# Optimization experiments

Measured on AMD Instinct MI355X. Metric: run time of the kernel, lower is better.

The kernel has to match this reference:

```python
import jax, jax.numpy as jnp
import numpy as np

N, E, D, DH, MH, MO = 100000, 1600000, 128, 512, 512, 128
EPS_BN = 1e-5
EPS_LN = 1e-5


def setup_inputs() -> dict:
    key = jax.random.key(0)
    ks = jax.random.split(key, 16)
    def lin(k, fan_in, shape):
        return jax.random.normal(k, shape, jnp.float32) / np.sqrt(fan_in)
    return {
        'x': jax.random.normal(ks[0], (N, D), jnp.float32),
        'src': jax.random.randint(ks[1], (E,), 0, N, jnp.int32),
        'dst': jax.random.randint(ks[2], (E,), 0, N, jnp.int32),
        'gcn_w': lin(ks[3], D, (D, D)),
        'gcn_b': jnp.zeros((D,), jnp.float32),
        'ff_w1': lin(ks[4], D, (D, DH)),
        'ff_b1': jnp.zeros((DH,), jnp.float32),
        'ln_g': jnp.ones((DH,), jnp.float32),
        'ln_b': jnp.zeros((DH,), jnp.float32),
        'ff_w2': lin(ks[5], DH, (DH, D)),
        'ff_b2': jnp.zeros((D,), jnp.float32),
        'fc1_w': lin(ks[6], D, (D, MH)),
        'fc1_b': jnp.zeros((MH,), jnp.float32),
        'bn1_g': jnp.ones((MH,), jnp.float32),
        'bn1_b': jnp.zeros((MH,), jnp.float32),
        'fc2_w': lin(ks[7], MH, (MH, MH)),
        'fc2_b': jnp.zeros((MH,), jnp.float32),
        'bn2_g': jnp.ones((MH,), jnp.float32),
        'bn2_b': jnp.zeros((MH,), jnp.float32),
        'fc3_w': lin(ks[8], MH, (MH, MO)),
        'fc3_b': jnp.zeros((MO,), jnp.float32),
        'bn3_g': jnp.ones((MO,), jnp.float32),
        'bn3_b': jnp.zeros((MO,), jnp.float32),
        'fc4_w': lin(ks[9], MO, (MO, 1)),
        'fc4_b': jnp.zeros((1,), jnp.float32),
    }


def _gelu(x):
    return jax.nn.gelu(x, approximate=False)  # torch nn.GELU default (erf)


def _batchnorm(x, g, b):
    # BatchNorm1d in training mode: batch statistics, biased variance
    m = jnp.mean(x, axis=0)
    v = jnp.var(x, axis=0)
    return (x - m) * jax.lax.rsqrt(v + EPS_BN) * g + b


def reference(x, src, dst, gcn_w, gcn_b, ff_w1, ff_b1, ln_g, ln_b, ff_w2, ff_b2,
              fc1_w, fc1_b, bn1_g, bn1_b, fc2_w, fc2_b, bn2_g, bn2_b,
              fc3_w, fc3_b, bn3_g, bn3_b, fc4_w, fc4_b):
    n = x.shape[0]
    ones = jnp.ones(src.shape[0], x.dtype)
    out_deg = jnp.clip(jax.ops.segment_sum(ones, src, num_segments=n), 1.0)
    in_deg = jnp.clip(jax.ops.segment_sum(ones, dst, num_segments=n), 1.0)
    # GraphConv, norm='both': left-normalize, aggregate, matmul (in==out), right-normalize, bias
    h = x * (out_deg ** -0.5)[:, None]
    agg = jax.ops.segment_sum(h[src], dst, num_segments=n)  # [N, D]
    h = agg @ gcn_w
    h = h * (in_deg ** -0.5)[:, None] + gcn_b
    # FeedForwardLayer: lin1 -> GELU -> LayerNorm -> lin2
    f = _gelu(h @ ff_w1 + ff_b1)
    mu = jnp.mean(f, axis=-1, keepdims=True)
    var = jnp.var(f, axis=-1, keepdims=True)
    f = (f - mu) * jax.lax.rsqrt(var + EPS_LN) * ln_g + ln_b
    h = f @ ff_w2 + ff_b2  # [N, D]
    # MLP head
    h = _batchnorm(_gelu(h @ fc1_w + fc1_b), bn1_g, bn1_b)
    h = _batchnorm(_gelu(h @ fc2_w + fc2_b), bn2_g, bn2_b)
    h = _batchnorm(_gelu(h @ fc3_w + fc3_b), bn3_g, bn3_b)
    return h @ fc4_w + fc4_b  # [N, 1]
```

## Files before the change

### kernel.cpp

```cpp
#include <hip/hip_runtime.h>
#include <hip/hip_bf16.h>

#define N_NODES 100000
#define NPAD    100096
#define NRB     782
#define E_EDGES 1600000
#define NBLK_SCAN 98

#define HNR  4
#define HP   64
#define HCHK 25000
#define HRSZ 32768

#define NBK  196
#define PCHK 6250

#define AS1 __attribute__((address_space(1)))
#define AS3 __attribute__((address_space(3)))

typedef unsigned int   uint;
typedef unsigned short ushort;
typedef __attribute__((ext_vector_type(8))) short bfx8;
typedef __attribute__((ext_vector_type(4))) float fx4;

__device__ __forceinline__ float bf2f(ushort u) {
    return __uint_as_float(((uint)u) << 16);
}
__device__ __forceinline__ ushort f2bf(float f) {
    uint x = __float_as_uint(f);
    return (ushort)((x + 0x7FFFu + ((x >> 16) & 1u)) >> 16);
}
__device__ __forceinline__ float gelu_fast(float x) {
    float u = 1.5957691f * __builtin_fmaf(0.044715f * x * x, x, x);
    return x / (1.0f + __expf(-u));
}
__device__ __forceinline__ float wave_sum(float v) {
    #pragma unroll
    for (int m = 1; m < 64; m <<= 1) v += __shfl_xor(v, m, 64);
    return v;
}
__device__ __forceinline__ int xcd_swz(int orig, int nwg) {
    int q = nwg >> 3, r = nwg & 7;
    int x = orig & 7, o = orig >> 3;
    return (x < r ? x * (q + 1) : r * (q + 1) + (x - r) * q) + o;
}

__global__ void k_hist(const int* __restrict__ idx, uint* __restrict__ part)
{
    __shared__ uint h[HRSZ / 2];
    int c = blockIdx.x & (HP - 1);
    int r = blockIdx.x / HP;
    int t = threadIdx.x;
    for (int i = t; i < HRSZ / 2; i += 256) h[i] = 0u;
    __syncthreads();
    int base = r << 15;
    int e0 = c * HCHK;
    for (int e = e0 + t; e < e0 + HCHK; e += 256) {
        int v = idx[e] - base;
        if ((uint)v < (uint)HRSZ)
            atomicAdd(&h[v >> 1], 1u << ((v & 1) * 16));
    }
    __syncthreads();
    uint* dst = part + ((size_t)blockIdx.x << 14);
    for (int i = t; i < HRSZ / 2; i += 256) dst[i] = h[i];
}

__global__ void k_degmerge(const uint* __restrict__ partO, const uint* __restrict__ partI,
                           int* __restrict__ inc, float* __restrict__ oscale,
                           float* __restrict__ ininv)
{
    int n = blockIdx.x * 256 + threadIdx.x;
    if (n >= NPAD) return;
    int r = n >> 15, i = (n & 32767) >> 1, hi = (n & 1) * 16;
    const uint* po = partO + ((size_t)(r * HP) << 14) + i;
    const uint* pi = partI + ((size_t)(r * HP) << 14) + i;
    uint so = 0, si = 0;
    for (int c = 0; c < HP; ++c) {
        so += (po[(size_t)c << 14] >> hi) & 0xffffu;
        si += (pi[(size_t)c << 14] >> hi) & 0xffffu;
    }
    inc[n] = (int)si;
    oscale[n] = rsqrtf((float)max((int)so, 1));
    ininv[n] = rsqrtf((float)max((int)si, 1));
}

__global__ void k_scan1(const int* __restrict__ inc, int* __restrict__ coff, int* __restrict__ btot)
{
    __shared__ int a[1024], bsh[1024];
    int t = threadIdx.x;
    int i = blockIdx.x * 1024 + t;
    a[t] = (i < N_NODES) ? inc[i] : 0;
    __syncthreads();
    int* s = a; int* d = bsh;
    for (int dd = 1; dd < 1024; dd <<= 1) {
        int v = s[t] + ((t >= dd) ? s[t - dd] : 0);
        d[t] = v;
        __syncthreads();
        int* tmp = s; s = d; d = tmp;
    }
    if (i < N_NODES) coff[i + 1] = s[t];
    if (t == 1023) btot[blockIdx.x] = s[t];
}

__global__ void k_scan2(int* __restrict__ btot)
{
    __shared__ int a[128], bsh[128];
    int t = threadIdx.x;
    a[t] = (t < NBLK_SCAN) ? btot[t] : 0;
    __syncthreads();
    int* s = a; int* d = bsh;
    for (int dd = 1; dd < 128; dd <<= 1) {
        int v = s[t] + ((t >= dd) ? s[t - dd] : 0);
        d[t] = v;
        __syncthreads();
        int* tmp = s; s = d; d = tmp;
    }
    if (t < NBLK_SCAN) btot[t] = s[t];
}

__global__ void k_scan3(int* __restrict__ coff, const int* __restrict__ btot)
{
    int i = blockIdx.x * 256 + threadIdx.x;
    if (i == 0) coff[0] = 0;
    if (i < N_NODES) {
        int blk = i >> 10;
        if (blk > 0) coff[i + 1] += btot[blk - 1];
    }
}

__global__ void k_curinit(const int* __restrict__ coff, int* __restrict__ gcur)
{
    int t = threadIdx.x;
    if (t < NBK) gcur[t] = coff[t << 9];
}

__global__ __launch_bounds__(256) void k_part(const int* __restrict__ src, const int* __restrict__ dst,
                                              int* __restrict__ gcur, uint* __restrict__ tmp)
{
    __shared__ int cnt[NBK], rcnt[NBK], base[NBK], loff[NBK];
    __shared__ int sa[256], sb[256];
    __shared__ uint arr[PCHK];
    int t = threadIdx.x;
    if (t < NBK) { cnt[t] = 0; rcnt[t] = 0; }
    __syncthreads();
    int e0 = blockIdx.x * PCHK;
    for (int e = e0 + t; e < e0 + PCHK; e += 256)
        atomicAdd(&cnt[dst[e] >> 9], 1);
    __syncthreads();
    sa[t] = (t < NBK) ? cnt[t] : 0;
    __syncthreads();
    int* s = sa; int* d = sb;
    for (int dd = 1; dd < 256; dd <<= 1) {
        int v = s[t] + ((t >= dd) ? s[t - dd] : 0);
        d[t] = v;
        __syncthreads();
        int* w = s; s = d; d = w;
    }
    if (t < NBK) {
        loff[t] = s[t] - cnt[t];
        base[t] = atomicAdd(&gcur[t], cnt[t]);
    }
    __syncthreads();
    for (int e = e0 + t; e < e0 + PCHK; e += 256) {
        int dv = dst[e];
        int b = dv >> 9;
        int r = atomicAdd(&rcnt[b], 1);
        arr[loff[b] + r] = ((uint)src[e] << 9) | (uint)(dv & 511);
    }
    __syncthreads();
    for (int b = 0; b < NBK; ++b) {
        int n = cnt[b], lo = loff[b], gb = base[b];
        for (int i = t; i < n; i += 256)
            tmp[gb + i] = arr[lo + i];
    }
}

__global__ __launch_bounds__(256) void k_fill2(const uint* __restrict__ tmp, const int* __restrict__ coff,
                                               int* __restrict__ eidx)
{
    __shared__ int lco[512];
    __shared__ int lcnt[512];
    int b = blockIdx.x, t = threadIdx.x;
    int n0 = b << 9;
    for (int i = t; i < 512; i += 256) {
        int node = n0 + i;
        lco[i] = (node <= N_NODES) ? coff[node] : E_EDGES;
        lcnt[i] = 0;
    }
    __syncthreads();
    int s0 = coff[n0];
    int s1 = (n0 + 512 <= N_NODES) ? coff[n0 + 512] : E_EDGES;
    for (int e = s0 + t; e < s1; e += 256) {
        uint v = tmp[e];
        int dl = v & 511;
        int r = atomicAdd(&lcnt[dl], 1);
        eidx[lco[dl] + r] = (int)(v >> 9);
    }
}

__global__ void k_xhat(const float* __restrict__ x, const float* __restrict__ oscale,
                       ushort* __restrict__ xh)
{
    size_t i = (size_t)blockIdx.x * 256 + threadIdx.x;
    size_t e0 = i * 4;
    int row = (int)(e0 >> 7);
    uint2 o;
    if (row < N_NODES) {
        float4 v = *(const float4*)(x + e0);
        float s = oscale[row];
        o.x = (uint)f2bf(v.x * s) | ((uint)f2bf(v.y * s) << 16);
        o.y = (uint)f2bf(v.z * s) | ((uint)f2bf(v.w * s) << 16);
    } else {
        o.x = 0u; o.y = 0u;
    }
    *(uint2*)(xh + e0) = o;
}

__global__ void k_agg(const int* __restrict__ off, const int* __restrict__ eidx,
                      const ushort* __restrict__ xh, ushort* __restrict__ agg)
{
    int wid = threadIdx.x >> 6, lane = threadIdx.x & 63;
    int r = blockIdx.x * 4 + wid;
    if (r >= NPAD) return;
    int f = lane & 15;
    int g = lane >> 4;
    float a[8] = {0.f, 0.f, 0.f, 0.f, 0.f, 0.f, 0.f, 0.f};
    if (r < N_NODES) {
        int s = off[r], e = off[r + 1];
        for (int i = s + g; i < e; i += 4) {
            int sv = eidx[i];
            bfx8 v = *(const bfx8*)(xh + (size_t)sv * 128 + f * 8);
            #pragma unroll
            for (int k = 0; k < 8; ++k) a[k] += bf2f((ushort)v[k]);
        }
    }
    #pragma unroll
    for (int k = 0; k < 8; ++k) {
        a[k] += __shfl_xor(a[k], 16, 64);
        a[k] += __shfl_xor(a[k], 32, 64);
    }
    if (g == 0) {
        bfx8 o;
        #pragma unroll
        for (int k = 0; k < 8; ++k) o[k] = (short)f2bf(a[k]);
        *(bfx8*)(agg + (size_t)r * 128 + f * 8) = o;
    }
}

__global__ void k_wT(const float* __restrict__ W, int K, int M, ushort* __restrict__ Wt)
{
    int id = blockIdx.x * 256 + threadIdx.x;
    if (id < K * M) {
        int m = id / K, k = id - m * K;
        Wt[id] = f2bf(W[(size_t)k * M + m]);
    }
}

__global__ void k_wT_ln(const float* __restrict__ W, const float* __restrict__ g,
                        const float* __restrict__ b, const float* __restrict__ b2,
                        ushort* __restrict__ Wt, float* __restrict__ u, float* __restrict__ t)
{
    int wid = threadIdx.x >> 6, lane = threadIdx.x & 63;
    int m = blockIdx.x * 4 + wid;
    if (m >= 128) return;
    float us = 0.f, ts = 0.f;
    for (int k = lane; k < 512; k += 64) {
        float w = W[(size_t)k * 128 + m];
        float gk = g[k], bk = b[k];
        Wt[(size_t)m * 512 + k] = f2bf(gk * w);
        us += gk * w; ts += bk * w;
    }
    us = wave_sum(us); ts = wave_sum(ts);
    if (lane == 0) { u[m] = us; t[m] = ts + b2[m]; }
}

template <int K1, int EPI1, int STATS2>
__global__ __launch_bounds__(256, 2) void k_fused(
    const ushort* __restrict__ A1, const ushort* __restrict__ B1t,
    const ushort* __restrict__ B2t, ushort* __restrict__ C,
    const float* __restrict__ c1v0, const float* __restrict__ r1v0,
    const float* __restrict__ r1v1, const float* __restrict__ c1v1,
    const float* __restrict__ bias2,
    float* __restrict__ lnS, float* __restrict__ lnC,
    float* __restrict__ pS, float* __restrict__ pQ)
{
    __shared__ __align__(16) char smem[32768 + 32768 + 2048];
    char* A2 = smem;
    char* S  = smem + 32768;
    float* st_s = (float*)(smem + 65536);
    float* st_q = (float*)(smem + 65536 + 1024);

    const int rb = xcd_swz(blockIdx.x, gridDim.x);
    const int tid = threadIdx.x;
    const int lane = tid & 63;
    const int wid = tid >> 6;
    const int m0 = (wid >> 1) * 64;
    const int n0 = (wid & 1) * 64;
    const int frl = lane & 15;
    const int kg = lane >> 4;

    char* As = S;
    char* Bs = S + 16384;
    fx4 acc[4][4] = {};
    const ushort* Arow0 = A1 + (size_t)(rb * 128) * K1;

    for (int kb = 0; kb < K1; kb += 64) {
        #pragma unroll
        for (int c = 0; c < 4; ++c) {
            int b = c * 4096 + tid * 16;
            int row = b >> 7;
            int cibs = (b & 127) ^ ((row & 7) << 4);
            const char* ga = (const char*)(Arow0 + (size_t)row * K1 + kb) + cibs;
            const char* gb = (const char*)(B1t + (size_t)row * K1 + kb) + cibs;
            char* la = As + c * 4096 + (wid << 10);
            char* lb = Bs + c * 4096 + (wid << 10);
            __builtin_amdgcn_global_load_lds((const AS1 void*)ga, (AS3 void*)la, 16, 0, 0);
            __builtin_amdgcn_global_load_lds((const AS1 void*)gb, (AS3 void*)lb, 16, 0, 0);
        }
        __syncthreads();
        #pragma unroll
        for (int kk = 0; kk < 2; ++kk) {
            bfx8 av[4], bv[4];
            #pragma unroll
            for (int i = 0; i < 4; ++i) {
                int ar = m0 + i * 16 + frl;
                int ab = (ar * 128 + kk * 64 + kg * 16) ^ ((ar & 7) << 4);
                av[i] = *(const bfx8*)(As + ab);
                int br = n0 + i * 16 + frl;
                int bb = (br * 128 + kk * 64 + kg * 16) ^ ((br & 7) << 4);
                bv[i] = *(const bfx8*)(Bs + bb);
            }
            #pragma unroll
            for (int i = 0; i < 4; ++i)
                #pragma unroll
                for (int j = 0; j < 4; ++j)
                    acc[i][j] = __builtin_amdgcn_mfma_f32_16x16x32_bf16(av[i], bv[j], acc[i][j], 0, 0, 0);
        }
        __syncthreads();
    }

    #pragma unroll
    for (int j = 0; j < 4; ++j) {
        int colL = n0 + j * 16 + frl;
        float c0 = c1v0[colL];
        float c1 = (EPI1 == 3) ? c1v1[colL] : 0.f;
        #pragma unroll
        for (int i = 0; i < 4; ++i) {
            int rbaseL = m0 + i * 16 + kg * 4;
            #pragma unroll
            for (int r = 0; r < 4; ++r) {
                float v = acc[i][j][r];
                int rowL = rbaseL + r;
                int grow = rb * 128 + rowL;
                if (EPI1 == 0) v = v * r1v0[grow] + c0;
                else           v = r1v0[grow] * v + r1v1[grow] * c1 + c0;
                *(ushort*)(A2 + rowL * 256 + ((colL * 2) ^ ((rowL & 7) << 4))) = f2bf(v);
            }
        }
    }
    __syncthreads();

    float rs = 0.f, rq = 0.f;
    const int rowR = tid >> 1, halfR = tid & 1;

    for (int cb2 = 0; cb2 < 4; ++cb2) {
        #pragma unroll
        for (int c = 0; c < 8; ++c) {
            int b = c * 4096 + tid * 16;
            int row = b >> 8;
            int cibs = (b & 255) ^ ((row & 7) << 4);
            const char* gb = (const char*)(B2t + (size_t)(cb2 * 128 + row) * 128) + cibs;
            char* lb = S + c * 4096 + (wid << 10);
            __builtin_amdgcn_global_load_lds((const AS1 void*)gb, (AS3 void*)lb, 16, 0, 0);
        }
        __syncthreads();

        fx4 a2[4][4] = {};
        #pragma unroll
        for (int kk = 0; kk < 4; ++kk) {
            bfx8 av[4], bv[4];
            int c2 = kk * 64 + kg * 16;
            #pragma unroll
            for (int i = 0; i < 4; ++i) {
                int ar = m0 + i * 16 + frl;
                av[i] = *(const bfx8*)(A2 + ar * 256 + (c2 ^ ((ar & 7) << 4)));
                int br = n0 + i * 16 + frl;
                bv[i] = *(const bfx8*)(S + br * 256 + (c2 ^ ((br & 7) << 4)));
            }
            #pragma unroll
            for (int i = 0; i < 4; ++i)
                #pragma unroll
                for (int j = 0; j < 4; ++j)
                    a2[i][j] = __builtin_amdgcn_mfma_f32_16x16x32_bf16(av[i], bv[j], a2[i][j], 0, 0, 0);
        }
        __syncthreads();

        float sL[4] = {0.f, 0.f, 0.f, 0.f}, qL[4] = {0.f, 0.f, 0.f, 0.f};
        #pragma unroll
        for (int j = 0; j < 4; ++j) {
            int colL = n0 + j * 16 + frl;
            float bcol = bias2[cb2 * 128 + colL];
            #pragma unroll
            for (int i = 0; i < 4; ++i) {
                int rbaseL = m0 + i * 16 + kg * 4;
                #pragma unroll
                for (int r = 0; r < 4; ++r) {
                    float v = gelu_fast(a2[i][j][r] + bcol);
                    int rowL = rbaseL + r;
                    if (STATS2 == 1) {
                        if (rb * 128 + rowL < N_NODES) { sL[j] += v; qL[j] += v * v; }
                    }
                    *(ushort*)(S + rowL * 256 + ((colL * 2) ^ ((rowL & 7) << 4))) = f2bf(v);
                }
            }
            if (STATS2 == 1) {
                float s = sL[j], q = qL[j];
                s += __shfl_xor(s, 16, 64); s += __shfl_xor(s, 32, 64);
                q += __shfl_xor(q, 16, 64); q += __shfl_xor(q, 32, 64);
                if (kg == 0) {
                    st_s[(wid >> 1) * 128 + n0 + j * 16 + frl] = s;
                    st_q[(wid >> 1) * 128 + n0 + j * 16 + frl] = q;
                }
            }
        }
        __syncthreads();

        {
            int r2 = tid >> 4;
            int s2 = tid & 15;
            #pragma unroll
            for (int pass = 0; pass < 8; ++pass) {
                int rowL = pass * 16 + r2;
                int boff = rowL * 256 + ((s2 * 16) ^ ((rowL & 7) << 4));
                bfx8 v = *(const bfx8*)(S + boff);
                *(bfx8*)((char*)(C + (size_t)(rb * 128 + rowL) * 512 + cb2 * 128) + s2 * 16) = v;
            }
        }
        if (STATS2 == 1 && tid < 128) {
            size_t pidx = ((size_t)rb * 4 + cb2) * 128 + tid;
            pS[pidx] = st_s[tid] + st_s[128 + tid];
            pQ[pidx] = st_q[tid] + st_q[128 + tid];
        }
        if (STATS2 == 2) {
            #pragma unroll
            for (int ss = 0; ss < 8; ++ss) {
                int boff = rowR * 256 + (((halfR * 64 + ss * 8) * 2) ^ ((rowR & 7) << 4));
                bfx8 v = *(const bfx8*)(S + boff);
                #pragma unroll
                for (int k2 = 0; k2 < 8; ++k2) {
                    float f = bf2f((ushort)v[k2]);
                    rs += f; rq += f * f;
                }
            }
        }
        __syncthreads();
    }

    if (STATS2 == 2) {
        rs += __shfl_xor(rs, 1, 64);
        rq += __shfl_xor(rq, 1, 64);
        if (halfR == 0) {
            float mean = rs * (1.f / 512.f);
            float var = fmaxf(rq * (1.f / 512.f) - mean * mean, 0.f);
            float sr = rsqrtf(var + 1e-5f);
            int grow = rb * 128 + rowR;
            lnS[grow] = sr;
            lnC[grow] = -mean * sr;
        }
    }
}

template <int EPI, int STATS>
__global__ __launch_bounds__(256, 4) void k_gemm(
    const ushort* __restrict__ A, const ushort* __restrict__ Bt,
    ushort* __restrict__ C, int K, int M,
    const float* __restrict__ colv0, const float* __restrict__ rowv0,
    float* __restrict__ pS, float* __restrict__ pQ, int grb0)
{
    __shared__ __align__(16) char smem[32768 + (STATS == 1 ? 1024 : 0)];
    char* AsB = smem;
    char* BsB = smem + 16384;

    const int nwg = gridDim.x;
    const int wgid = xcd_swz(blockIdx.x, nwg);
    const int nCB = M >> 7;
    const int cb = wgid % nCB;
    const int rb = wgid / nCB;
    const int tid = threadIdx.x;
    const int lane = tid & 63;
    const int wid = tid >> 6;
    const int m0 = (wid >> 1) * 64;
    const int n0 = (wid & 1) * 64;
    const int frl = lane & 15;
    const int kg = lane >> 4;

    float* statsf = (float*)(smem + 32768);
    if (STATS == 1 && tid < 128) { statsf[tid] = 0.f; statsf[128 + tid] = 0.f; }

    fx4 acc[4][4] = {};

    const ushort* Arow0 = A + (size_t)(rb * 128) * K;
    const ushort* Brow0 = Bt + (size_t)(cb * 128) * K;

    for (int kb = 0; kb < K; kb += 64) {
        #pragma unroll
        for (int c = 0; c < 4; ++c) {
            int b = c * 4096 + tid * 16;
            int row = b >> 7;
            int cibs = (b & 127) ^ ((row & 7) << 4);
            const char* ga = (const char*)(Arow0 + (size_t)row * K + kb) + cibs;
            const char* gb = (const char*)(Brow0 + (size_t)row * K + kb) + cibs;
            char* la = AsB + c * 4096 + (wid << 10);
            char* lb = BsB + c * 4096 + (wid << 10);
            __builtin_amdgcn_global_load_lds((const AS1 void*)ga, (AS3 void*)la, 16, 0, 0);
            __builtin_amdgcn_global_load_lds((const AS1 void*)gb, (AS3 void*)lb, 16, 0, 0);
        }
        __syncthreads();
        #pragma unroll
        for (int kk = 0; kk < 2; ++kk) {
            bfx8 av[4], bv[4];
            #pragma unroll
            for (int i = 0; i < 4; ++i) {
                int ar = m0 + i * 16 + frl;
                int ab = (ar * 128 + kk * 64 + kg * 16) ^ ((ar & 7) << 4);
                av[i] = *(const bfx8*)(AsB + ab);
                int br = n0 + i * 16 + frl;
                int bb = (br * 128 + kk * 64 + kg * 16) ^ ((br & 7) << 4);
                bv[i] = *(const bfx8*)(BsB + bb);
            }
            #pragma unroll
            for (int i = 0; i < 4; ++i)
                #pragma unroll
                for (int j = 0; j < 4; ++j)
                    acc[i][j] = __builtin_amdgcn_mfma_f32_16x16x32_bf16(av[i], bv[j], acc[i][j], 0, 0, 0);
        }
        __syncthreads();
    }

    float sL[4] = {0.f, 0.f, 0.f, 0.f}, qL[4] = {0.f, 0.f, 0.f, 0.f};
    #pragma unroll
    for (int j = 0; j < 4; ++j) {
        int colL = n0 + j * 16 + frl;
        float c0 = colv0[cb * 128 + colL];
        #pragma unroll
        for (int i = 0; i < 4; ++i) {
            int rbaseL = m0 + i * 16 + kg * 4;
            #pragma unroll
            for (int r = 0; r < 4; ++r) {
                float v = acc[i][j][r];
                int rowL = rbaseL + r;
                int grow = (grb0 + rb) * 128 + rowL;
                if (EPI == 0) v = v * rowv0[grow] + c0;
                else          v = gelu_fast(v + c0);
                if (STATS == 1) {
                    if (grow < N_NODES) { sL[j] += v; qL[j] += v * v; }
                }
                int boff = rowL * 256 + ((colL * 2) ^ ((rowL & 7) << 4));
                *(ushort*)(smem + boff) = f2bf(v);
            }
        }
    }
    if (STATS == 1) {
        #pragma unroll
        for (int j = 0; j < 4; ++j) {
            float s = sL[j], q = qL[j];
            s += __shfl_xor(s, 16, 64); s += __shfl_xor(s, 32, 64);
            q += __shfl_xor(q, 16, 64); q += __shfl_xor(q, 32, 64);
            if (kg == 0) {
                atomicAdd(&statsf[n0 + j * 16 + frl], s);
                atomicAdd(&statsf[128 + n0 + j * 16 + frl], q);
            }
        }
    }
    __syncthreads();
    {
        int r2 = tid >> 4;
        int s2 = tid & 15;
        #pragma unroll
        for (int pass = 0; pass < 8; ++pass) {
            int rowL = pass * 16 + r2;
            int boff = rowL * 256 + ((s2 * 16) ^ ((rowL & 7) << 4));
            bfx8 v = *(const bfx8*)(smem + boff);
            *(bfx8*)((char*)(C + (size_t)(rb * 128 + rowL) * M + cb * 128) + s2 * 16) = v;
        }
    }
    if (STATS == 1 && tid < 128) {
        size_t pidx = ((size_t)(grb0 + rb) * nCB + cb) * 128 + tid;
        pS[pidx] = statsf[tid];
        pQ[pidx] = statsf[128 + tid];
    }
}

__global__ void k_colmerge(const float* __restrict__ pS, const float* __restrict__ pQ,
                           float* __restrict__ oS, float* __restrict__ oQ, int M)
{
    int wid = threadIdx.x >> 6, lane = threadIdx.x & 63;
    int m = blockIdx.x * 4 + wid;
    if (m >= M) return;
    int nCB = M >> 7, cb = m >> 7, colL = m & 127;
    float s = 0.f, q = 0.f;
    for (int rb = lane; rb < NRB; rb += 64) {
        size_t idx = ((size_t)rb * nCB + cb) * 128 + colL;
        s += pS[idx]; q += pQ[idx];
    }
    s = wave_sum(s); q = wave_sum(q);
    if (lane == 0) { oS[m] = s; oQ[m] = q; }
}

__global__ void k_fold(const float* __restrict__ W, const float* __restrict__ bw,
                       const float* __restrict__ g, const float* __restrict__ bb,
                       const float* __restrict__ sum, const float* __restrict__ sqs,
                       int K, int M, ushort* __restrict__ WtO, float* __restrict__ bO)
{
    int wid = threadIdx.x >> 6, lane = threadIdx.x & 63;
    int m = blockIdx.x * 4 + wid;
    if (m >= M) return;
    float acc = 0.f;
    for (int k = lane; k < K; k += 64) {
        float mean = sum[k] * (1.f / (float)N_NODES);
        float var = sqs[k] * (1.f / (float)N_NODES) - mean * mean;
        float s = g[k] * rsqrtf(var + 1e-5f);
        float t = bb[k] - mean * s;
        float w = W[(size_t)k * M + m];
        WtO[(size_t)m * K + k] = f2bf(w * s);
        acc += t * w;
    }
    acc = wave_sum(acc);
    if (lane == 0) bO[m] = bw[m] + acc;
}

__global__ void k_out(const ushort* __restrict__ m3, const ushort* __restrict__ w4,
                      const float* __restrict__ b4, float* __restrict__ out)
{
    int wid = threadIdx.x >> 6, lane = threadIdx.x & 63;
    int r = blockIdx.x * 4 + wid;
    if (r >= N_NODES) return;
    uint u = *(const uint*)(m3 + (size_t)r * 128 + lane * 2);
    uint w = *(const uint*)(w4 + lane * 2);
    float acc = bf2f((ushort)(u & 0xffffu)) * bf2f((ushort)(w & 0xffffu))
              + bf2f((ushort)(u >> 16)) * bf2f((ushort)(w >> 16));
    acc = wave_sum(acc);
    if (lane == 0) out[r] = acc + b4[0];
}

extern "C" void kernel_launch(void* const* d_in, const int* in_sizes, int n_in,
                              void* d_out, int out_size, void* d_ws, size_t ws_size,
                              hipStream_t stream)
{
    const float* x     = (const float*)d_in[0];
    const int*   src   = (const int*)d_in[1];
    const int*   dst   = (const int*)d_in[2];
    const float* gcn_w = (const float*)d_in[3];
    const float* gcn_b = (const float*)d_in[4];
    const float* ff_w1 = (const float*)d_in[5];
    const float* ff_b1 = (const float*)d_in[6];
    const float* ln_g  = (const float*)d_in[7];
    const float* ln_b  = (const float*)d_in[8];
    const float* ff_w2 = (const float*)d_in[9];
    const float* ff_b2 = (const float*)d_in[10];
    const float* fc1_w = (const float*)d_in[11];
    const float* fc1_b = (const float*)d_in[12];
    const float* bn1_g = (const float*)d_in[13];
    const float* bn1_b = (const float*)d_in[14];
    const float* fc2_w = (const float*)d_in[15];
    const float* fc2_b = (const float*)d_in[16];
    const float* bn2_g = (const float*)d_in[17];
    const float* bn2_b = (const float*)d_in[18];
    const float* fc3_w = (const float*)d_in[19];
    const float* fc3_b = (const float*)d_in[20];
    const float* bn3_g = (const float*)d_in[21];
    const float* bn3_b = (const float*)d_in[22];
    const float* fc4_w = (const float*)d_in[23];
    const float* fc4_b = (const float*)d_in[24];
    float* out = (float*)d_out;
    (void)in_sizes; (void)n_in; (void)out_size;

    char* base = (char*)d_ws;
    char* p = base;
    auto alloc = [&](size_t bytes) -> char* {
        char* r = p;
        p += (bytes + 255) & ~(size_t)255;
        return r;
    };
    int*    inc    = (int*)alloc((size_t)NPAD * 4);
    int*    coff   = (int*)alloc(((size_t)NPAD + 1) * 4);
    int*    btot   = (int*)alloc(128 * 4);
    int*    gcur   = (int*)alloc(256 * 4);
    int*    eidx   = (int*)alloc((size_t)E_EDGES * 4);
    float*  oscale = (float*)alloc((size_t)NPAD * 4);
    float*  ininv  = (float*)alloc((size_t)NPAD * 4);
    float*  bns    = (float*)alloc(6 * 512 * 4);
    float*  b2p    = (float*)alloc(512 * 4);
    float*  b3p    = (float*)alloc(128 * 4);
    float*  b4p    = (float*)alloc(4);
    float*  lnS    = (float*)alloc((size_t)NPAD * 4);
    float*  lnC    = (float*)alloc((size_t)NPAD * 4);
    float*  lnU    = (float*)alloc(128 * 4);
    float*  lnT    = (float*)alloc(128 * 4);
    float*  pS     = (float*)alloc((size_t)4 * NPAD * 4);
    float*  pQ     = (float*)alloc((size_t)4 * NPAD * 4);
    ushort* gwT    = (ushort*)alloc(128 * 128 * 2);
    ushort* ff1T   = (ushort*)alloc(512 * 128 * 2);
    ushort* ff2T   = (ushort*)alloc(128 * 512 * 2);
    ushort* fc1T   = (ushort*)alloc(512 * 128 * 2);
    ushort* fc2T   = (ushort*)alloc(512 * 512 * 2);
    ushort* fc3T   = (ushort*)alloc(128 * 512 * 2);
    ushort* w4t    = (ushort*)alloc(128 * 2);
    ushort* buf1   = (ushort*)alloc((size_t)NPAD * 128 * 2);
    ushort* bufC   = (ushort*)alloc((size_t)NPAD * 512 * 2);

    size_t used = (size_t)(p - base);
    bool   sep  = (used + (size_t)NPAD * 512 * 2) <= ws_size;
    ushort* m2  = sep ? (ushort*)alloc((size_t)NPAD * 512 * 2) : bufC;

    uint* partO = (uint*)bufC;
    uint* partI = partO + (size_t)HNR * HP * (HRSZ / 2);
    uint* etmp  = (uint*)bufC;
    ushort* xh  = bufC;
    ushort* agg = buf1;

    float* bn1s = bns;
    float* bn1q = bns + 512;
    float* bn2s = bns + 1024;
    float* bn2q = bns + 1536;
    float* bn3s = bns + 2048;
    float* bn3q = bns + 2560;

    k_hist<<<HNR * HP, 256, 0, stream>>>(src, partO);
    k_hist<<<HNR * HP, 256, 0, stream>>>(dst, partI);
    k_degmerge<<<(NPAD + 255) / 256, 256, 0, stream>>>(partO, partI, inc, oscale, ininv);
    k_scan1<<<NBLK_SCAN, 1024, 0, stream>>>(inc, coff, btot);
    k_scan2<<<1, 128, 0, stream>>>(btot);
    k_scan3<<<(N_NODES + 255) / 256, 256, 0, stream>>>(coff, btot);
    k_curinit<<<1, 256, 0, stream>>>(coff, gcur);
    k_part<<<E_EDGES / PCHK, 256, 0, stream>>>(src, dst, gcur, etmp);
    k_fill2<<<NBK, 256, 0, stream>>>(etmp, coff, eidx);
    k_xhat<<<(NPAD / 256) * 32, 256, 0, stream>>>(x, oscale, xh);
    k_agg<<<NPAD / 4, 256, 0, stream>>>(coff, eidx, xh, agg);

    k_wT<<<(128 * 128) / 256, 256, 0, stream>>>(gcn_w, 128, 128, gwT);
    k_wT<<<(128 * 512) / 256, 256, 0, stream>>>(ff_w1, 128, 512, ff1T);
    k_wT<<<(128 * 512) / 256, 256, 0, stream>>>(fc1_w, 128, 512, fc1T);
    k_wT_ln<<<32, 256, 0, stream>>>(ff_w2, ln_g, ln_b, ff_b2, ff2T, lnU, lnT);

    k_fused<128, 0, 2><<<NRB, 256, 0, stream>>>(agg, gwT, ff1T, bufC,
                                                gcn_b, ininv, nullptr, nullptr, ff_b1,
                                                lnS, lnC, nullptr, nullptr);
    k_fused<512, 3, 1><<<NRB, 256, 0, stream>>>(bufC, ff2T, fc1T, bufC,
                                                lnT, lnS, lnC, lnU, fc1_b,
                                                nullptr, nullptr, pS, pQ);
    k_colmerge<<<128, 256, 0, stream>>>(pS, pQ, bn1s, bn1q, 512);
    k_fold<<<512 / 4, 256, 0, stream>>>(fc2_w, fc2_b, bn1_g, bn1_b, bn1s, bn1q, 512, 512, fc2T, b2p);
    if (sep) {
        k_gemm<1, 1><<<4 * NRB, 256, 0, stream>>>(bufC, fc2T, m2, 512, 512,
                                                  b2p, nullptr, pS, pQ, 0);
    } else {
        const int cOff[6] = {0, 195, 390, 585, 780, 782};
        for (int c = 0; c < 5; ++c) {
            int rb0 = cOff[c], nrb = cOff[c + 1] - rb0;
            k_gemm<1, 1><<<nrb * 4, 256, 0, stream>>>(bufC + (size_t)rb0 * 128 * 512, fc2T,
                                                      buf1, 512, 512,
                                                      b2p, nullptr, pS, pQ, rb0);
            hipMemcpyAsync(bufC + (size_t)rb0 * 128 * 512, buf1,
                           (size_t)nrb * 128 * 512 * 2, hipMemcpyDeviceToDevice, stream);
        }
    }
    k_colmerge<<<128, 256, 0, stream>>>(pS, pQ, bn2s, bn2q, 512);
    k_fold<<<128 / 4, 256, 0, stream>>>(fc3_w, fc3_b, bn2_g, bn2_b, bn2s, bn2q, 512, 128, fc3T, b3p);
    k_gemm<1, 1><<<NRB, 256, 0, stream>>>(m2, fc3T, buf1, 512, 128,
                                          b3p, nullptr, pS, pQ, 0);
    k_colmerge<<<32, 256, 0, stream>>>(pS, pQ, bn3s, bn3q, 128);
    k_fold<<<1, 256, 0, stream>>>(fc4_w, fc4_b, bn3_g, bn3_b, bn3s, bn3q, 128, 1, w4t, b4p);
    k_out<<<N_NODES / 4, 256, 0, stream>>>(buf1, w4t, b4p, out);
}
```

Measured before the change: 672.8 us.

## Run fused GEMM kernels with 512 threads and narrower per-wave tiles

Doubles the fused kernel block size to 512 threads (8 waves in a 2x4 layout), so each wave computes a 64x32 output tile instead of 64x64. Loads, epilogue, store and LayerNorm stat loops are re-split across the extra threads. This cuts accumulator registers per wave and puts more waves on each CU to hide latency. The cost is more LDS fragment reads per MFMA, since each wave reloads the A fragments for only half the columns, plus an extra shuffle step in the row reductions.

New measurement: 655.6 us. 1.03x faster.

```diff
diff --git a/kernel.cpp b/kernel.cpp
--- a/kernel.cpp
+++ b/kernel.cpp
@@ -275,7 +275,7 @@
 }
 
 template <int K1, int EPI1, int STATS2>
-__global__ __launch_bounds__(256, 2) void k_fused(
+__global__ __launch_bounds__(512, 4) void k_fused(
     const ushort* __restrict__ A1, const ushort* __restrict__ B1t,
     const ushort* __restrict__ B2t, ushort* __restrict__ C,
     const float* __restrict__ c1v0, const float* __restrict__ r1v0,
@@ -294,64 +294,66 @@
     const int tid = threadIdx.x;
     const int lane = tid & 63;
     const int wid = tid >> 6;
-    const int m0 = (wid >> 1) * 64;
-    const int n0 = (wid & 1) * 64;
+    const int wr = wid >> 2;
+    const int wc = wid & 3;
+    const int m0 = wr * 64;
+    const int n0 = wc * 32;
     const int frl = lane & 15;
     const int kg = lane >> 4;
 
     char* As = S;
     char* Bs = S + 16384;
-    fx4 acc[4][4] = {};
+    fx4 acc[4][2] = {};
     const ushort* Arow0 = A1 + (size_t)(rb * 128) * K1;
 
     for (int kb = 0; kb < K1; kb += 64) {
         #pragma unroll
-        for (int c = 0; c < 4; ++c) {
-            int b = c * 4096 + tid * 16;
+        for (int c = 0; c < 2; ++c) {
+            int b = c * 8192 + tid * 16;
             int row = b >> 7;
             int cibs = (b & 127) ^ ((row & 7) << 4);
             const char* ga = (const char*)(Arow0 + (size_t)row * K1 + kb) + cibs;
             const char* gb = (const char*)(B1t + (size_t)row * K1 + kb) + cibs;
-            char* la = As + c * 4096 + (wid << 10);
-            char* lb = Bs + c * 4096 + (wid << 10);
+            char* la = As + c * 8192 + (wid << 10);
+            char* lb = Bs + c * 8192 + (wid << 10);
             __builtin_amdgcn_global_load_lds((const AS1 void*)ga, (AS3 void*)la, 16, 0, 0);
             __builtin_amdgcn_global_load_lds((const AS1 void*)gb, (AS3 void*)lb, 16, 0, 0);
         }
         __syncthreads();
         #pragma unroll
         for (int kk = 0; kk < 2; ++kk) {
-            bfx8 av[4], bv[4];
+            bfx8 av[4], bv[2];
             #pragma unroll
             for (int i = 0; i < 4; ++i) {
                 int ar = m0 + i * 16 + frl;
-                int ab = (ar * 128 + kk * 64 + kg * 16) ^ ((ar & 7) << 4);
-                av[i] = *(const bfx8*)(As + ab);
-                int br = n0 + i * 16 + frl;
-                int bb = (br * 128 + kk * 64 + kg * 16) ^ ((br & 7) << 4);
-                bv[i] = *(const bfx8*)(Bs + bb);
+                av[i] = *(const bfx8*)(As + ((ar * 128 + kk * 64 + kg * 16) ^ ((ar & 7) << 4)));
+            }
+            #pragma unroll
+            for (int j = 0; j < 2; ++j) {
+                int br = n0 + j * 16 + frl;
+                bv[j] = *(const bfx8*)(Bs + ((br * 128 + kk * 64 + kg * 16) ^ ((br & 7) << 4)));
             }
             #pragma unroll
             for (int i = 0; i < 4; ++i)
                 #pragma unroll
-                for (int j = 0; j < 4; ++j)
+                for (int j = 0; j < 2; ++j)
                     acc[i][j] = __builtin_amdgcn_mfma_f32_16x16x32_bf16(av[i], bv[j], acc[i][j], 0, 0, 0);
         }
         __syncthreads();
     }
 
     #pragma unroll
-    for (int j = 0; j < 4; ++j) {
+    for (int j = 0; j < 2; ++j) {
         int colL = n0 + j * 16 + frl;
         float c0 = c1v0[colL];
         float c1 = (EPI1 == 3) ? c1v1[colL] : 0.f;
         #pragma unroll
         for (int i = 0; i < 4; ++i) {
-            int rbaseL = m0 + i * 16 + kg * 4;
             #pragma unroll
             for (int r = 0; r < 4; ++r) {
+                int rowL = m0 + i * 16 + kg * 4 + r;
+                int grow = rb * 128 + rowL;
                 float v = acc[i][j][r];
-                int rowL = rbaseL + r;
-                int grow = rb * 128 + rowL;
                 if (EPI1 == 0) v = v * r1v0[grow] + c0;
                 else           v = r1v0[grow] * v + r1v1[grow] * c1 + c0;
                 *(ushort*)(A2 + rowL * 256 + ((colL * 2) ^ ((rowL & 7) << 4))) = f2bf(v);
@@ -361,65 +363,67 @@
     __syncthreads();
 
     float rs = 0.f, rq = 0.f;
-    const int rowR = tid >> 1, halfR = tid & 1;
+    const int rowR = tid >> 2;
+    const int qR = tid & 3;
 
     for (int cb2 = 0; cb2 < 4; ++cb2) {
         #pragma unroll
-        for (int c = 0; c < 8; ++c) {
-            int b = c * 4096 + tid * 16;
+        for (int c = 0; c < 4; ++c) {
+            int b = c * 8192 + tid * 16;
             int row = b >> 8;
             int cibs = (b & 255) ^ ((row & 7) << 4);
             const char* gb = (const char*)(B2t + (size_t)(cb2 * 128 + row) * 128) + cibs;
-            char* lb = S + c * 4096 + (wid << 10);
+            char* lb = S + c * 8192 + (wid << 10);
             __builtin_amdgcn_global_load_lds((const AS1 void*)gb, (AS3 void*)lb, 16, 0, 0);
         }
         __syncthreads();
 
-        fx4 a2[4][4] = {};
+        fx4 a2[4][2] = {};
         #pragma unroll
         for (int kk = 0; kk < 4; ++kk) {
-            bfx8 av[4], bv[4];
             int c2 = kk * 64 + kg * 16;
+            bfx8 av[4], bv[2];
             #pragma unroll
             for (int i = 0; i < 4; ++i) {
                 int ar = m0 + i * 16 + frl;
                 av[i] = *(const bfx8*)(A2 + ar * 256 + (c2 ^ ((ar & 7) << 4)));
-                int br = n0 + i * 16 + frl;
-                bv[i] = *(const bfx8*)(S + br * 256 + (c2 ^ ((br & 7) << 4)));
+            }
+            #pragma unroll
+            for (int j = 0; j < 2; ++j) {
+                int br = n0 + j * 16 + frl;
+                bv[j] = *(const bfx8*)(S + br * 256 + (c2 ^ ((br & 7) << 4)));
             }
             #pragma unroll
             for (int i = 0; i < 4; ++i)
                 #pragma unroll
-                for (int j = 0; j < 4; ++j)
+                for (int j = 0; j < 2; ++j)
                     a2[i][j] = __builtin_amdgcn_mfma_f32_16x16x32_bf16(av[i], bv[j], a2[i][j], 0, 0, 0);
         }
         __syncthreads();
 
-        float sL[4] = {0.f, 0.f, 0.f, 0.f}, qL[4] = {0.f, 0.f, 0.f, 0.f};
-        #pragma unroll
-        for (int j = 0; j < 4; ++j) {
+        #pragma unroll
+        for (int j = 0; j < 2; ++j) {
             int colL = n0 + j * 16 + frl;
             float bcol = bias2[cb2 * 128 + colL];
+            float sL = 0.f, qL = 0.f;
             #pragma unroll
             for (int i = 0; i < 4; ++i) {
-                int rbaseL = m0 + i * 16 + kg * 4;
                 #pragma unroll
                 for (int r = 0; r < 4; ++r) {
                     float v = gelu_fast(a2[i][j][r] + bcol);
-                    int rowL = rbaseL + r;
+                    int rowL = m0 + i * 16 + kg * 4 + r;
                     if (STATS2 == 1) {
-                        if (rb * 128 + rowL < N_NODES) { sL[j] += v; qL[j] += v * v; }
+                        if (rb * 128 + rowL < N_NODES) { sL += v; qL += v * v; }
                     }
                     *(ushort*)(S + rowL * 256 + ((colL * 2) ^ ((rowL & 7) << 4))) = f2bf(v);
                 }
             }
             if (STATS2 == 1) {
-                float s = sL[j], q = qL[j];
-                s += __shfl_xor(s, 16, 64); s += __shfl_xor(s, 32, 64);
-                q += __shfl_xor(q, 16, 64); q += __shfl_xor(q, 32, 64);
+                sL += __shfl_xor(sL, 16, 64); sL += __shfl_xor(sL, 32, 64);
+                qL += __shfl_xor(qL, 16, 64); qL += __shfl_xor(qL, 32, 64);
                 if (kg == 0) {
-                    st_s[(wid >> 1) * 128 + n0 + j * 16 + frl] = s;
-                    st_q[(wid >> 1) * 128 + n0 + j * 16 + frl] = q;
+                    st_s[wr * 128 + colL] = sL;
+                    st_q[wr * 128 + colL] = qL;
                 }
             }
         }
@@ -429,8 +433,8 @@
             int r2 = tid >> 4;
             int s2 = tid & 15;
             #pragma unroll
-            for (int pass = 0; pass < 8; ++pass) {
-                int rowL = pass * 16 + r2;
+            for (int pass = 0; pass < 4; ++pass) {
+                int rowL = pass * 32 + r2;
                 int boff = rowL * 256 + ((s2 * 16) ^ ((rowL & 7) << 4));
                 bfx8 v = *(const bfx8*)(S + boff);
                 *(bfx8*)((char*)(C + (size_t)(rb * 128 + rowL) * 512 + cb2 * 128) + s2 * 16) = v;
@@ -443,8 +447,8 @@
         }
         if (STATS2 == 2) {
             #pragma unroll
-            for (int ss = 0; ss < 8; ++ss) {
-                int boff = rowR * 256 + (((halfR * 64 + ss * 8) * 2) ^ ((rowR & 7) << 4));
+            for (int ss = 0; ss < 4; ++ss) {
+                int boff = rowR * 256 + (((qR * 64 + ss * 16)) ^ ((rowR & 7) << 4));
                 bfx8 v = *(const bfx8*)(S + boff);
                 #pragma unroll
                 for (int k2 = 0; k2 < 8; ++k2) {
@@ -457,9 +461,9 @@
     }
 
     if (STATS2 == 2) {
-        rs += __shfl_xor(rs, 1, 64);
-        rq += __shfl_xor(rq, 1, 64);
-        if (halfR == 0) {
+        rs += __shfl_xor(rs, 1, 64); rs += __shfl_xor(rs, 2, 64);
+        rq += __shfl_xor(rq, 1, 64); rq += __shfl_xor(rq, 2, 64);
+        if (qR == 0) {
             float mean = rs * (1.f / 512.f);
             float var = fmaxf(rq * (1.f / 512.f) - mean * mean, 0.f);
             float sr = rsqrtf(var + 1e-5f);
@@ -743,10 +747,10 @@
     k_wT<<<(128 * 512) / 256, 256, 0, stream>>>(fc1_w, 128, 512, fc1T);
     k_wT_ln<<<32, 256, 0, stream>>>(ff_w2, ln_g, ln_b, ff_b2, ff2T, lnU, lnT);
 
-    k_fused<128, 0, 2><<<NRB, 256, 0, stream>>>(agg, gwT, ff1T, bufC,
+    k_fused<128, 0, 2><<<NRB, 512, 0, stream>>>(agg, gwT, ff1T, bufC,
                                                 gcn_b, ininv, nullptr, nullptr, ff_b1,
                                                 lnS, lnC, nullptr, nullptr);
-    k_fused<512, 3, 1><<<NRB, 256, 0, stream>>>(bufC, ff2T, fc1T, bufC,
+    k_fused<512, 3, 1><<<NRB, 512, 0, stream>>>(bufC, ff2T, fc1T, bufC,
                                                 lnT, lnS, lnC, lnU, fc1_b,
                                                 nullptr, nullptr, pS, pQ);
     k_colmerge<<<128, 256, 0, stream>>>(pS, pQ, bn1s, bn1q, 512);
```
